# Kernel tuning notes

Hardware: AMD Instinct MI355X
Metric: run time of the kernel (lower is better)

Reference implementation:

```python
import jax, jax.numpy as jnp
import numpy as np

B, N, E, F, U = 256, 240, 4338, 28, 100
NEG_SLOPE = 0.2  # PyG GATConv default negative_slope


def setup_inputs() -> dict:
    key = jax.random.key(0)
    ks = jax.random.split(key, 13)
    s = 0.05  # xavier-ish scale
    return {
        "inputs": jax.random.normal(ks[0], (B, N * F), jnp.float32),
        "state": jax.random.normal(ks[1], (B, N * U), jnp.float32),
        "edge_src": jax.random.randint(ks[2], (E,), 0, N, jnp.int32),
        "edge_dst": jax.random.randint(ks[3], (E,), 0, N, jnp.int32),
        # GATConv(U+F -> U): linear weight, attention vectors, output bias
        "Wg": jax.random.normal(ks[4], (U, U + F), jnp.float32) * s,
        "att_src": jax.random.normal(ks[5], (U,), jnp.float32) * s,
        "att_dst": jax.random.normal(ks[6], (U,), jnp.float32) * s,
        "gat_bias": jnp.zeros((U,), jnp.float32),
        # bias_1 added in _gc3 (self.biases[(100,)])
        "bias1": jnp.zeros((U,), jnp.float32),
        # GRU1: GRULinear(100, 200); GRU2: GRULinear(100, 100)
        "W_ru": jax.random.normal(ks[7], (U + F, 2 * U), jnp.float32) * s,
        "b_ru": jnp.zeros((2 * U,), jnp.float32),
        "W_c": jax.random.normal(ks[8], (U + F, U), jnp.float32) * s,
        "b_c": jnp.zeros((U,), jnp.float32),
    }


def _gat_gru(inputs, state, src, dst, Wg, att_src, att_dst, gat_bias, bias1,
             W_ru, b_ru, W_c, b_c):
    xi = inputs.reshape(B, N, F)
    xs = state.reshape(B, N, U)
    # _gc3: concat [state, inputs] -> GATConv per sample (vectorized here)
    x = jnp.concatenate([xs, xi], axis=2)                 # [B, N, U+F]
    h = jnp.einsum("bnf,cf->bnc", x, Wg)                  # [B, N, U]
    a_src = h @ att_src                                    # [B, N]
    a_dst = h @ att_dst                                    # [B, N]
    e = jax.nn.leaky_relu(a_src[:, src] + a_dst[:, dst], NEG_SLOPE)  # [B, E+N]
    eT = e.T                                               # [E+N, B]
    emax = jax.ops.segment_max(eT, dst, num_segments=N)    # [N, B]
    ex = jnp.exp(eT - emax[dst])
    denom = jax.ops.segment_sum(ex, dst, num_segments=N)   # [N, B]
    alpha = ex / denom[dst]                                # [E+N, B]
    msgs = h[:, src].transpose(1, 0, 2) * alpha[:, :, None]  # [E+N, B, U]
    agg = jax.ops.segment_sum(msgs, dst, num_segments=N)   # [N, B, U]
    gstate = agg.transpose(1, 0, 2) + gat_bias + bias1     # [B, N, U]
    st = gstate.reshape(B, N * U)
    # GRU gates (GRULinear concatenates [inputs, hidden] on feature dim)
    cat1 = jnp.concatenate([xi, gstate], axis=2).reshape(-1, U + F)
    ru = jax.nn.sigmoid((cat1 @ W_ru + b_ru).reshape(B, N, 2 * U))
    r = ru[..., :U].reshape(B, N * U)
    u = ru[..., U:].reshape(B, N * U)
    cat2 = jnp.concatenate([xi, (r * st).reshape(B, N, U)], axis=2).reshape(-1, U + F)
    c = jnp.tanh(cat2 @ W_c + b_c).reshape(B, N * U)
    return u * st + (1.0 - u) * c


def reference(inputs, state, edge_src, edge_dst, Wg, att_src, att_dst,
              gat_bias, bias1, W_ru, b_ru, W_c, b_c):
    # PyG GATConv default add_self_loops=True
    loops = jnp.arange(N, dtype=edge_src.dtype)
    src = jnp.concatenate([edge_src, loops])
    dst = jnp.concatenate([edge_dst, loops])
    return _gat_gru(inputs, state, src, dst, Wg, att_src, att_dst, gat_bias,
                    bias1, W_ru, b_ru, W_c, b_c)
```

## Files before the change

### kernel.cpp

```cpp
#include <hip/hip_runtime.h>

#define Bb 256
#define Nn 240
#define Ee 4338
#define Ff 28
#define Uu 100
#define Kk 128
#define ET (Ee + Nn)
#define AS 136

typedef __attribute__((ext_vector_type(8))) short bf16x8;
typedef __attribute__((ext_vector_type(4))) float f32x4;
typedef unsigned short u16;

__device__ __forceinline__ float bf2f(u16 u) {
  union { unsigned int i; float f; } v; v.i = ((unsigned int)u) << 16; return v.f;
}
__device__ __forceinline__ u16 f2bf(float f) {
  union { float ff; unsigned int i; } v; v.ff = f;
  unsigned int x = v.i;
  return (u16)((x + 0x7fffu + ((x >> 16) & 1u)) >> 16);
}
__device__ __forceinline__ void split4(const float4 v, ushort4& h, ushort4& l) {
  u16 h0 = f2bf(v.x), h1 = f2bf(v.y), h2 = f2bf(v.z), h3 = f2bf(v.w);
  h.x = h0; h.y = h1; h.z = h2; h.w = h3;
  l.x = f2bf(v.x - bf2f(h0)); l.y = f2bf(v.y - bf2f(h1));
  l.z = f2bf(v.z - bf2f(h2)); l.w = f2bf(v.w - bf2f(h3));
}
__device__ __forceinline__ bf16x8 pack8(ushort4 a, ushort4 b) {
  bf16x8 r;
  r[0] = (short)a.x; r[1] = (short)a.y; r[2] = (short)a.z; r[3] = (short)a.w;
  r[4] = (short)b.x; r[5] = (short)b.y; r[6] = (short)b.z; r[7] = (short)b.w;
  return r;
}

__global__ __launch_bounds__(512, 2) void k_fused(
    const float* __restrict__ stt, const float* __restrict__ inp,
    const float* __restrict__ Wg,
    const float* __restrict__ att_s, const float* __restrict__ att_d,
    const int* __restrict__ esrc, const int* __restrict__ edst,
    const float* __restrict__ gbias, const float* __restrict__ b1,
    const float* __restrict__ Wru, const float* __restrict__ bru,
    const float* __restrict__ Wc, const float* __restrict__ bc,
    float* __restrict__ out) {
  __shared__ float hbuf[Nn * Uu];
  __shared__ u16 ahL[32 * AS];
  __shared__ u16 alL[32 * AS];
  __shared__ float gch[32 * Uu];
  __shared__ u16 ugQ[32 * Uu];
  __shared__ float asrcL[Nn];
  __shared__ float adstL[Nn];
  __shared__ int coffL[Nn + 1];
  __shared__ int cslotL[ET];
  __shared__ int curL[Nn];
  __shared__ int scanA[256];

  int tid = threadIdx.x;
  int b = blockIdx.x;
  const size_t sbase = (size_t)b * Nn * Uu;
  const size_t ibase = (size_t)b * Nn * Ff;

  if (tid < 256) scanA[tid] = 0;
  for (int i = tid; i < Nn; i += 512) { asrcL[i] = 0.f; adstL[i] = 0.f; }
  __syncthreads();
  for (int e = tid; e < Ee; e += 512) atomicAdd(&scanA[edst[e]], 1);
  __syncthreads();
  int xv = 0, incl = 0;
  if (tid < 256) {
    xv = (tid < Nn) ? (scanA[tid] + 1) : 0;
    incl = xv;
  }
  __syncthreads();
  if (tid < 256) scanA[tid] = incl;
  __syncthreads();
#pragma unroll
  for (int d = 1; d < 256; d <<= 1) {
    int t = 0;
    if (tid < 256 && tid >= d) t = scanA[tid - d];
    __syncthreads();
    if (tid < 256) { incl += t; scanA[tid] = incl; }
    __syncthreads();
  }
  if (tid < 256) {
    int excl = incl - xv;
    if (tid < Nn) { coffL[tid] = excl; curL[tid] = excl; }
    if (tid == 0) coffL[Nn] = scanA[Nn - 1];
  }
  __syncthreads();
  for (int e = tid; e < Ee; e += 512) {
    int d = edst[e];
    cslotL[atomicAdd(&curL[d], 1)] = esrc[e];
  }
  for (int n = tid; n < Nn; n += 512) cslotL[atomicAdd(&curL[n], 1)] = n;

  int w = tid >> 6, l = tid & 63, l15 = l & 15, q = l >> 4;
  int cw = w * 16 + l15;
  int llb = l & 31, half = l >> 5;

  float4 gbv = {0.f, 0.f, 0.f, 0.f};
  if (l < 25) {
    int u0 = l * 4;
    gbv.x = gbias[u0 + 0] + b1[u0 + 0];
    gbv.y = gbias[u0 + 1] + b1[u0 + 1];
    gbv.z = gbias[u0 + 2] + b1[u0 + 2];
    gbv.w = gbias[u0 + 3] + b1[u0 + 3];
  }

  f32x4 zero = {0.f, 0.f, 0.f, 0.f};

  {
    bf16x8 wh[4], wl[4];
#pragma unroll
    for (int s = 0; s < 4; ++s) {
      float4 v0 = {0.f, 0.f, 0.f, 0.f}, v1 = {0.f, 0.f, 0.f, 0.f};
      if (cw < Uu) {
        v0 = *(const float4*)(Wg + cw * Kk + s * 32 + q * 8);
        v1 = *(const float4*)(Wg + cw * Kk + s * 32 + q * 8 + 4);
      }
      ushort4 h0, l0, h1, l1;
      split4(v0, h0, l0);
      split4(v1, h1, l1);
      wh[s] = pack8(h0, h1);
      wl[s] = pack8(l0, l1);
    }
    float av = (cw < Uu) ? att_s[cw] : 0.f;
    float dv = (cw < Uu) ? att_d[cw] : 0.f;

    for (int ch0 = 0; ch0 < Nn; ch0 += 32) {
      int rows = Nn - ch0; if (rows > 32) rows = 32;
      int nrt = rows >> 4;
      for (int j = tid; j < rows * 32; j += 512) {
        int r = j >> 5, g = j & 31;
        float4 v = (g < 25)
            ? *(const float4*)(stt + sbase + (size_t)(ch0 + r) * Uu + g * 4)
            : *(const float4*)(inp + ibase + (size_t)(ch0 + r) * Ff + (g - 25) * 4);
        ushort4 hh, lo;
        split4(v, hh, lo);
        *(ushort4*)(ahL + r * AS + g * 4) = hh;
        *(ushort4*)(alL + r * AS + g * 4) = lo;
      }
      __syncthreads();
      f32x4 acc[2]; acc[0] = zero; acc[1] = zero;
#pragma unroll
      for (int rt = 0; rt < 2; ++rt) if (rt < nrt) {
#pragma unroll
        for (int s = 0; s < 4; ++s) {
          bf16x8 a = *(const bf16x8*)(ahL + (rt * 16 + l15) * AS + s * 32 + q * 8);
          bf16x8 bb = *(const bf16x8*)(alL + (rt * 16 + l15) * AS + s * 32 + q * 8);
          acc[rt] = __builtin_amdgcn_mfma_f32_16x16x32_bf16(a, wh[s], acc[rt], 0, 0, 0);
          acc[rt] = __builtin_amdgcn_mfma_f32_16x16x32_bf16(bb, wh[s], acc[rt], 0, 0, 0);
          acc[rt] = __builtin_amdgcn_mfma_f32_16x16x32_bf16(a, wl[s], acc[rt], 0, 0, 0);
        }
      }
#pragma unroll
      for (int rt = 0; rt < 2; ++rt) if (rt < nrt) {
#pragma unroll
        for (int i = 0; i < 4; ++i) {
          float v = acc[rt][i];
          int row = rt * 16 + q * 4 + i;
          if (cw < Uu) hbuf[(ch0 + row) * Uu + cw] = v;
          float va = v * av, vd = v * dv;
#pragma unroll
          for (int msk = 1; msk < 16; msk <<= 1) {
            va += __shfl_xor(va, msk, 64);
            vd += __shfl_xor(vd, msk, 64);
          }
          if (l15 == 0) {
            atomicAdd(&asrcL[ch0 + row], va);
            atomicAdd(&adstL[ch0 + row], vd);
          }
        }
      }
      __syncthreads();
    }
  }

  bf16x8 r0h[4], r0l[4], r1h[4], r1l[4], cch[4], ccl[4];
  int cw1 = 128 + cw;
#pragma unroll
  for (int s = 0; s < 4; ++s) {
    int kb = s * 32 + q * 8;
#pragma unroll
    for (int j = 0; j < 8; ++j) {
      int kp = kb + j;
      int k = (kp < Uu) ? (kp + Ff) : (kp - Uu);
      float v0 = Wru[k * (2 * Uu) + cw];
      u16 h0 = f2bf(v0);
      r0h[s][j] = (short)h0; r0l[s][j] = (short)f2bf(v0 - bf2f(h0));
      float v1 = (cw1 < 2 * Uu) ? Wru[k * (2 * Uu) + cw1] : 0.f;
      u16 h1 = f2bf(v1);
      r1h[s][j] = (short)h1; r1l[s][j] = (short)f2bf(v1 - bf2f(h1));
      float v2 = (cw < Uu) ? Wc[k * Uu + cw] : 0.f;
      u16 h2 = f2bf(v2);
      cch[s][j] = (short)h2; ccl[s][j] = (short)f2bf(v2 - bf2f(h2));
    }
  }
  float bru0 = bru[cw];
  float bru1 = (cw1 < 2 * Uu) ? bru[cw1] : 0.f;
  float bcv = (cw < Uu) ? bc[cw] : 0.f;

  for (int ch0 = 0; ch0 < Nn; ch0 += 32) {
    int rows = Nn - ch0; if (rows > 32) rows = 32;
    int nrt = rows >> 4;

    for (int n = ch0 + w; n < ch0 + rows; n += 8) {
      int o0 = coffL[n], deg = coffL[n + 1] - o0;
      float ad = adstL[n];
      float ax = 0.f, ay = 0.f, az = 0.f, aw2 = 0.f, den = 0.f;
      for (int c0 = 0; c0 < deg; c0 += 64) {
        int e = c0 + l;
        float we = 0.f; int s = 0;
        if (e < deg) {
          s = cslotL[o0 + e];
          float sc = asrcL[s] + ad;
          sc = (sc > 0.f) ? sc : 0.2f * sc;
          we = __expf(sc);
        }
        float d = we;
#pragma unroll
        for (int msk = 1; msk < 64; msk <<= 1) d += __shfl_xor(d, msk, 64);
        den += d;
        int cn = deg - c0; if (cn > 64) cn = 64;
        for (int e2 = 0; e2 < cn; e2 += 2) {
          int eh = e2 + half;
          float w2 = __shfl(we, eh, 64);
          int s2 = __shfl(s, eh, 64);
          if ((llb < 25) && eh < cn) {
            const float4 hv = *(const float4*)(hbuf + s2 * Uu + llb * 4);
            ax += w2 * hv.x; ay += w2 * hv.y; az += w2 * hv.z; aw2 += w2 * hv.w;
          }
        }
      }
      ax += __shfl_xor(ax, 32, 64);
      ay += __shfl_xor(ay, 32, 64);
      az += __shfl_xor(az, 32, 64);
      aw2 += __shfl_xor(aw2, 32, 64);
      if (l < 25) {
        float inv = 1.f / den;
        float4 o;
        o.x = ax * inv + gbv.x;
        o.y = ay * inv + gbv.y;
        o.z = az * inv + gbv.z;
        o.w = aw2 * inv + gbv.w;
        *(float4*)(gch + (n - ch0) * Uu + l * 4) = o;
      }
    }
    __syncthreads();

    for (int j = tid; j < rows * 32; j += 512) {
      int r = j >> 5, g = j & 31;
      float4 v = (g < 25)
          ? *(const float4*)(gch + r * Uu + g * 4)
          : *(const float4*)(inp + ibase + (size_t)(ch0 + r) * Ff + (g - 25) * 4);
      ushort4 hh, lo;
      split4(v, hh, lo);
      *(ushort4*)(ahL + r * AS + g * 4) = hh;
      *(ushort4*)(alL + r * AS + g * 4) = lo;
    }
    float sv[2][4];
#pragma unroll
    for (int rt = 0; rt < 2; ++rt) if (rt < nrt) {
#pragma unroll
      for (int i = 0; i < 4; ++i) {
        int row = rt * 16 + q * 4 + i;
        sv[rt][i] = (cw < Uu) ? gch[row * Uu + cw] : 0.f;
      }
    }
    __syncthreads();

    float pr[2][4];
    {
      f32x4 acc[2]; acc[0] = zero; acc[1] = zero;
#pragma unroll
      for (int rt = 0; rt < 2; ++rt) if (rt < nrt) {
#pragma unroll
        for (int s = 0; s < 4; ++s) {
          bf16x8 a = *(const bf16x8*)(ahL + (rt * 16 + l15) * AS + s * 32 + q * 8);
          bf16x8 bb = *(const bf16x8*)(alL + (rt * 16 + l15) * AS + s * 32 + q * 8);
          acc[rt] = __builtin_amdgcn_mfma_f32_16x16x32_bf16(a, r0h[s], acc[rt], 0, 0, 0);
          acc[rt] = __builtin_amdgcn_mfma_f32_16x16x32_bf16(bb, r0h[s], acc[rt], 0, 0, 0);
          acc[rt] = __builtin_amdgcn_mfma_f32_16x16x32_bf16(a, r0l[s], acc[rt], 0, 0, 0);
        }
      }
#pragma unroll
      for (int rt = 0; rt < 2; ++rt) if (rt < nrt) {
#pragma unroll
        for (int i = 0; i < 4; ++i) {
          int row = rt * 16 + q * 4 + i;
          float y = acc[rt][i] + bru0;
          float g = 1.f / (1.f + __expf(-y));
          if (cw < Uu) pr[rt][i] = g * sv[rt][i];
          else ugQ[row * Uu + (cw - Uu)] = (u16)(g * 65535.f + 0.5f);
        }
      }
    }
    {
      f32x4 acc[2]; acc[0] = zero; acc[1] = zero;
#pragma unroll
      for (int rt = 0; rt < 2; ++rt) if (rt < nrt) {
#pragma unroll
        for (int s = 0; s < 4; ++s) {
          bf16x8 a = *(const bf16x8*)(ahL + (rt * 16 + l15) * AS + s * 32 + q * 8);
          bf16x8 bb = *(const bf16x8*)(alL + (rt * 16 + l15) * AS + s * 32 + q * 8);
          acc[rt] = __builtin_amdgcn_mfma_f32_16x16x32_bf16(a, r1h[s], acc[rt], 0, 0, 0);
          acc[rt] = __builtin_amdgcn_mfma_f32_16x16x32_bf16(bb, r1h[s], acc[rt], 0, 0, 0);
          acc[rt] = __builtin_amdgcn_mfma_f32_16x16x32_bf16(a, r1l[s], acc[rt], 0, 0, 0);
        }
      }
#pragma unroll
      for (int rt = 0; rt < 2; ++rt) if (rt < nrt) {
#pragma unroll
        for (int i = 0; i < 4; ++i) {
          int row = rt * 16 + q * 4 + i;
          float y = acc[rt][i] + bru1;
          float g = 1.f / (1.f + __expf(-y));
          if (cw1 < 2 * Uu) ugQ[row * Uu + (cw1 - Uu)] = (u16)(g * 65535.f + 0.5f);
        }
      }
    }
    __syncthreads();

#pragma unroll
    for (int rt = 0; rt < 2; ++rt) if (rt < nrt) {
#pragma unroll
      for (int i = 0; i < 4; ++i) {
        int row = rt * 16 + q * 4 + i;
        if (cw < Uu) {
          float p = pr[rt][i];
          u16 hh = f2bf(p);
          ahL[row * AS + cw] = hh;
          alL[row * AS + cw] = f2bf(p - bf2f(hh));
        }
      }
    }
    __syncthreads();

    {
      f32x4 acc[2]; acc[0] = zero; acc[1] = zero;
#pragma unroll
      for (int rt = 0; rt < 2; ++rt) if (rt < nrt) {
#pragma unroll
        for (int s = 0; s < 4; ++s) {
          bf16x8 a = *(const bf16x8*)(ahL + (rt * 16 + l15) * AS + s * 32 + q * 8);
          bf16x8 bb = *(const bf16x8*)(alL + (rt * 16 + l15) * AS + s * 32 + q * 8);
          acc[rt] = __builtin_amdgcn_mfma_f32_16x16x32_bf16(a, cch[s], acc[rt], 0, 0, 0);
          acc[rt] = __builtin_amdgcn_mfma_f32_16x16x32_bf16(bb, cch[s], acc[rt], 0, 0, 0);
          acc[rt] = __builtin_amdgcn_mfma_f32_16x16x32_bf16(a, ccl[s], acc[rt], 0, 0, 0);
        }
      }
#pragma unroll
      for (int rt = 0; rt < 2; ++rt) if (rt < nrt) {
#pragma unroll
        for (int i = 0; i < 4; ++i) {
          int row = rt * 16 + q * 4 + i;
          if (cw < Uu) {
            float y = acc[rt][i] + bcv;
            float cv = 1.f - 2.f / (__expf(2.f * y) + 1.f);
            float u = (float)ugQ[row * Uu + cw] * (1.f / 65535.f);
            out[sbase + (size_t)(ch0 + row) * Uu + cw] = u * sv[rt][i] + (1.f - u) * cv;
          }
        }
      }
    }
  }
}

extern "C" void kernel_launch(void* const* d_in, const int* in_sizes, int n_in,
                              void* d_out, int out_size, void* d_ws, size_t ws_size,
                              hipStream_t stream) {
  const float* inp   = (const float*)d_in[0];
  const float* stt   = (const float*)d_in[1];
  const int*   esrc  = (const int*)d_in[2];
  const int*   edst  = (const int*)d_in[3];
  const float* Wg    = (const float*)d_in[4];
  const float* att_s = (const float*)d_in[5];
  const float* att_d = (const float*)d_in[6];
  const float* gbias = (const float*)d_in[7];
  const float* b1    = (const float*)d_in[8];
  const float* Wru   = (const float*)d_in[9];
  const float* bru   = (const float*)d_in[10];
  const float* Wc    = (const float*)d_in[11];
  const float* bc    = (const float*)d_in[12];
  float* out = (float*)d_out;

  k_fused<<<Bb, 512, 0, stream>>>(stt, inp, Wg, att_s, att_d, esrc, edst,
                                  gbias, b1, Wru, bru, Wc, bc, out);
}
```

Before: 220.1 us.

## Replace block-wide scan with single-wave shuffle scan and overlap first chunk staging

Replaces the barrier-heavy 256-thread shared-memory prefix scan over in-degree counts with a warp-shuffle scan done by wave 0, while the other waves stage the first input chunk. CSR construction is overlapped with the first GEMM chunk, and staging of each later chunk moves to the end of the previous iteration. The goal is to cut the many __syncthreads in the prologue and hide setup latency. The chunk loop keeps the same number of barriers, and wave 0 sits idle during the first staging.

Result: no change. 218.0 us (-1.0%).

```diff
diff --git a/kernel.cpp b/kernel.cpp
--- a/kernel.cpp
+++ b/kernel.cpp
@@ -53,62 +53,37 @@
   __shared__ int coffL[Nn + 1];
   __shared__ int cslotL[ET];
   __shared__ int curL[Nn];
-  __shared__ int scanA[256];
+  __shared__ int cntA[Nn];
 
   int tid = threadIdx.x;
   int b = blockIdx.x;
   const size_t sbase = (size_t)b * Nn * Uu;
   const size_t ibase = (size_t)b * Nn * Ff;
 
-  if (tid < 256) scanA[tid] = 0;
-  for (int i = tid; i < Nn; i += 512) { asrcL[i] = 0.f; adstL[i] = 0.f; }
-  __syncthreads();
-  for (int e = tid; e < Ee; e += 512) atomicAdd(&scanA[edst[e]], 1);
-  __syncthreads();
-  int xv = 0, incl = 0;
-  if (tid < 256) {
-    xv = (tid < Nn) ? (scanA[tid] + 1) : 0;
-    incl = xv;
-  }
-  __syncthreads();
-  if (tid < 256) scanA[tid] = incl;
-  __syncthreads();
-#pragma unroll
-  for (int d = 1; d < 256; d <<= 1) {
-    int t = 0;
-    if (tid < 256 && tid >= d) t = scanA[tid - d];
-    __syncthreads();
-    if (tid < 256) { incl += t; scanA[tid] = incl; }
-    __syncthreads();
-  }
-  if (tid < 256) {
-    int excl = incl - xv;
-    if (tid < Nn) { coffL[tid] = excl; curL[tid] = excl; }
-    if (tid == 0) coffL[Nn] = scanA[Nn - 1];
-  }
-  __syncthreads();
-  for (int e = tid; e < Ee; e += 512) {
-    int d = edst[e];
-    cslotL[atomicAdd(&curL[d], 1)] = esrc[e];
-  }
-  for (int n = tid; n < Nn; n += 512) cslotL[atomicAdd(&curL[n], 1)] = n;
-
   int w = tid >> 6, l = tid & 63, l15 = l & 15, q = l >> 4;
   int cw = w * 16 + l15;
   int llb = l & 31, half = l >> 5;
 
-  float4 gbv = {0.f, 0.f, 0.f, 0.f};
-  if (l < 25) {
-    int u0 = l * 4;
-    gbv.x = gbias[u0 + 0] + b1[u0 + 0];
-    gbv.y = gbias[u0 + 1] + b1[u0 + 1];
-    gbv.z = gbias[u0 + 2] + b1[u0 + 2];
-    gbv.w = gbias[u0 + 3] + b1[u0 + 3];
-  }
-
   f32x4 zero = {0.f, 0.f, 0.f, 0.f};
 
+  auto stageChunk = [&](int c0, int rowsn, int base, int stride) {
+    for (int j = base; j < rowsn * 32; j += stride) {
+      int r = j >> 5, g = j & 31;
+      float4 v = (g < 25)
+          ? *(const float4*)(stt + sbase + (size_t)(c0 + r) * Uu + g * 4)
+          : *(const float4*)(inp + ibase + (size_t)(c0 + r) * Ff + (g - 25) * 4);
+      ushort4 hh, lo;
+      split4(v, hh, lo);
+      *(ushort4*)(ahL + r * AS + g * 4) = hh;
+      *(ushort4*)(alL + r * AS + g * 4) = lo;
+    }
+  };
+
   {
+    for (int i = tid; i < Nn; i += 512) { cntA[i] = 0; asrcL[i] = 0.f; adstL[i] = 0.f; }
+    __syncthreads();
+
+    for (int e = tid; e < Ee; e += 512) atomicAdd(&cntA[edst[e]], 1);
     bf16x8 wh[4], wl[4];
 #pragma unroll
     for (int s = 0; s < 4; ++s) {
@@ -125,21 +100,42 @@
     }
     float av = (cw < Uu) ? att_s[cw] : 0.f;
     float dv = (cw < Uu) ? att_d[cw] : 0.f;
+    __syncthreads();
+
+    if (w == 0) {
+      int carry = 0;
+#pragma unroll
+      for (int seg = 0; seg < 4; ++seg) {
+        int idx = seg * 64 + l;
+        int x = (idx < Nn) ? (cntA[idx] + 1) : 0;
+        int v = x;
+#pragma unroll
+        for (int d = 1; d < 64; d <<= 1) {
+          int t = __shfl_up(v, d, 64);
+          if (l >= d) v += t;
+        }
+        if (idx < Nn) {
+          int excl = carry + v - x;
+          coffL[idx] = excl;
+          curL[idx] = excl;
+        }
+        carry += __shfl(v, 63, 64);
+      }
+      if (l == 0) coffL[Nn] = carry;
+    } else {
+      stageChunk(0, 32, tid - 64, 448);
+    }
+    __syncthreads();
+
+    for (int e = tid; e < Ee; e += 512) {
+      int d = edst[e];
+      cslotL[atomicAdd(&curL[d], 1)] = esrc[e];
+    }
+    for (int n = tid; n < Nn; n += 512) cslotL[atomicAdd(&curL[n], 1)] = n;
 
     for (int ch0 = 0; ch0 < Nn; ch0 += 32) {
       int rows = Nn - ch0; if (rows > 32) rows = 32;
       int nrt = rows >> 4;
-      for (int j = tid; j < rows * 32; j += 512) {
-        int r = j >> 5, g = j & 31;
-        float4 v = (g < 25)
-            ? *(const float4*)(stt + sbase + (size_t)(ch0 + r) * Uu + g * 4)
-            : *(const float4*)(inp + ibase + (size_t)(ch0 + r) * Ff + (g - 25) * 4);
-        ushort4 hh, lo;
-        split4(v, hh, lo);
-        *(ushort4*)(ahL + r * AS + g * 4) = hh;
-        *(ushort4*)(alL + r * AS + g * 4) = lo;
-      }
-      __syncthreads();
       f32x4 acc[2]; acc[0] = zero; acc[1] = zero;
 #pragma unroll
       for (int rt = 0; rt < 2; ++rt) if (rt < nrt) {
@@ -172,7 +168,22 @@
         }
       }
       __syncthreads();
-    }
+      int nx = ch0 + 32;
+      if (nx < Nn) {
+        int rowsn = Nn - nx; if (rowsn > 32) rowsn = 32;
+        stageChunk(nx, rowsn, tid, 512);
+      }
+      __syncthreads();
+    }
+  }
+
+  float4 gbv = {0.f, 0.f, 0.f, 0.f};
+  if (l < 25) {
+    int u0 = l * 4;
+    gbv.x = gbias[u0 + 0] + b1[u0 + 0];
+    gbv.y = gbias[u0 + 1] + b1[u0 + 1];
+    gbv.z = gbias[u0 + 2] + b1[u0 + 2];
+    gbv.w = gbias[u0 + 3] + b1[u0 + 3];
   }
 
   bf16x8 r0h[4], r0l[4], r1h[4], r1l[4], cch[4], ccl[4];
```
